# Kernel tuning notes

Measured on AMD Instinct MI355X. Metric: run time of the kernel, lower is better.

## Reference

```python
import jax, jax.numpy as jnp
import numpy as np

N = 200000
C_IN = 128
C_OUT = 256
MID = C_OUT // 4  # bottleneck expansion = 4
K = 27            # 3x3x3 octree neighborhood
EPS = 1e-3


def setup_inputs() -> dict:
    key = jax.random.key(0)
    ks = jax.random.split(key, 8)
    x = jax.random.normal(ks[0], (N, C_IN), dtype=jnp.float32)
    neigh = jax.random.randint(ks[1], (N, K), 0, N, dtype=jnp.int32)
    w1 = jax.random.normal(ks[2], (C_IN, MID), dtype=jnp.float32) / np.sqrt(C_IN)
    w2 = jax.random.normal(ks[3], (K, MID, MID), dtype=jnp.float32) / np.sqrt(K * MID)
    w3 = jax.random.normal(ks[4], (MID, C_OUT), dtype=jnp.float32) / np.sqrt(MID)
    wp = jax.random.normal(ks[5], (C_IN, C_OUT), dtype=jnp.float32) / np.sqrt(C_IN)
    g1 = jnp.ones((MID,), jnp.float32);  b1 = jnp.zeros((MID,), jnp.float32)
    g2 = jnp.ones((MID,), jnp.float32);  b2 = jnp.zeros((MID,), jnp.float32)
    g3 = jnp.ones((C_OUT,), jnp.float32); b3 = jnp.zeros((C_OUT,), jnp.float32)
    gp = jnp.ones((C_OUT,), jnp.float32); bp = jnp.zeros((C_OUT,), jnp.float32)
    return {"x": x, "neigh": neigh, "depth": 6,
            "w1": w1, "g1": g1, "b1": b1,
            "w2": w2, "g2": g2, "b2": b2,
            "w3": w3, "g3": g3, "b3": b3,
            "wp": wp, "gp": gp, "bp": bp}


def _bn(h, g, b):
    # BatchNorm1d over node dim (training-mode batch stats, population var)
    m = jnp.mean(h, axis=0)
    v = jnp.var(h, axis=0)
    return (h - m) * jax.lax.rsqrt(v + EPS) * g + b


def reference(x, neigh, depth, w1, g1, b1, w2, g2, b2, w3, g3, b3, wp, gp, bp):
    # conv_bn_relu1: 1x1x1 octree conv (per-node linear) + BN + ReLU
    h = jax.nn.relu(_bn(x @ w1, g1, b1))           # [N, MID]
    # conv_bn_relu2: 3x3x3 octree conv = gather 27 neighbors + contract
    hn = h[neigh]                                   # [N, 27, MID] irregular gather
    h = jnp.einsum('nkc,kco->no', hn, w2)           # [N, MID]
    h = jax.nn.relu(_bn(h, g2, b2))
    # conv3 + bn3
    h = _bn(h @ w3, g3, b3)                         # [N, C_OUT]
    # projection branch
    p = _bn(x @ wp, gp, bp)                         # [N, C_OUT]
    return jax.nn.relu(h + p)
```

## Files before the change

kernel.cpp:

```cpp
#include <hip/hip_runtime.h>


typedef __bf16 bf16_8 __attribute__((ext_vector_type(8)));
typedef float f32x4 __attribute__((ext_vector_type(4)));

#define NN 200000
#define NBLK 3125

#define OFF_WA    (size_t)0
#define OFF_W3S   (size_t)81920
#define OFF_W2S   (size_t)114688
#define OFF_Y1    (size_t)335872
#define OFF_P1    (size_t)25935872
#define OFF_P2    (size_t)57935872
#define OFF_Y2    (size_t)64335872
#define OFF_H2B   (size_t)89935872
#define OFF_P3    (size_t)115535872
#define OFF_COEF  (size_t)141135872
#define OFF_PA1   (size_t)141142016
#define OFF_PA2   (size_t)141462016
#define OFF_PA3   (size_t)141526016


#define GLDS(gptr, lptr) __builtin_amdgcn_global_load_lds( \
    (const __attribute__((address_space(1))) unsigned int*)(gptr), \
    (__attribute__((address_space(3))) unsigned int*)(lptr), 16, 0, 0)

__global__ void k_prep(const float* __restrict__ w1, const float* __restrict__ w2,
                       const float* __restrict__ w3, const float* __restrict__ wp,
                       __bf16* __restrict__ wA, __bf16* __restrict__ w2S,
                       __bf16* __restrict__ w3S) {
    int i = blockIdx.x * 256 + threadIdx.x;
    if (i < 40960) {
        int j = i & 7, ln = (i >> 3) & 63, ks = (i >> 9) & 3, nt = i >> 11;
        int r = ks * 32 + (ln >> 4) * 8 + j;
        if (nt < 4) wA[i] = (__bf16)w1[r * 64 + nt * 16 + (ln & 15)];
        else        wA[i] = (__bf16)wp[r * 256 + (nt - 4) * 16 + (ln & 15)];
    }
    if (i < 16384) {
        int j = i & 7, ln = (i >> 3) & 63, ks = (i >> 9) & 1, nt = i >> 10;
        int r = ks * 32 + (ln >> 4) * 8 + j;
        w3S[i] = (__bf16)w3[r * 256 + nt * 16 + (ln & 15)];
    }
    if (i < 110592) {
        int j = i & 7, ln = (i >> 3) & 63, ks = (i >> 9) & 1, nt = (i >> 10) & 3, k = i >> 12;
        int c = ks * 32 + (ln >> 4) * 8 + j;
        int o = nt * 16 + (ln & 15);
        w2S[i] = (__bf16)w2[(k * 64 + c) * 64 + o];
    }
}

__global__ __launch_bounds__(256) void k1(const float* __restrict__ x,
                                          const __bf16* __restrict__ wA,
                                          __bf16* __restrict__ y1,
                                          float* __restrict__ p1) {
    __shared__ __align__(16) __bf16 bs[20480];
    __shared__ __align__(16) __bf16 yl[64][72];
    int blk = blockIdx.x, tid = threadIdx.x;
    int wave = tid >> 6, lane = tid & 63, l15 = lane & 15, lg = lane >> 4;

#pragma unroll
    for (int r = 0; r < 10; r++) {
        const char* g = (const char*)wA + r * 4096 + wave * 1024 + lane * 16;
        char* l = (char*)bs + r * 4096 + wave * 1024;
        GLDS(g, l);
    }

    int row = blk * 64 + wave * 16 + l15;
    const float* xr = x + (size_t)row * 128 + lg * 8;
    bf16_8 a[4];
#pragma unroll
    for (int ks = 0; ks < 4; ks++) {
        float4 f0 = *(const float4*)(xr + ks * 32);
        float4 f1 = *(const float4*)(xr + ks * 32 + 4);
        bf16_8 t;
        t[0] = (__bf16)f0.x; t[1] = (__bf16)f0.y; t[2] = (__bf16)f0.z; t[3] = (__bf16)f0.w;
        t[4] = (__bf16)f1.x; t[5] = (__bf16)f1.y; t[6] = (__bf16)f1.z; t[7] = (__bf16)f1.w;
        a[ks] = t;
    }

    f32x4 acc[20];
#pragma unroll
    for (int nt = 0; nt < 20; nt++) acc[nt] = (f32x4){0.f, 0.f, 0.f, 0.f};

    __syncthreads();
#pragma unroll
    for (int nt = 0; nt < 10; nt++) {
#pragma unroll
        for (int ks = 0; ks < 4; ks++) {
            bf16_8 b = *(const bf16_8*)(bs + ((nt * 4 + ks) * 64 + lane) * 8);
            acc[nt] = __builtin_amdgcn_mfma_f32_16x16x32_bf16(a[ks], b, acc[nt], 0, 0, 0);
        }
    }
    __syncthreads();

#pragma unroll
    for (int r = 0; r < 10; r++) {
        const char* g = (const char*)wA + 40960 + r * 4096 + wave * 1024 + lane * 16;
        char* l = (char*)bs + r * 4096 + wave * 1024;
        GLDS(g, l);
    }
#pragma unroll
    for (int nt = 0; nt < 4; nt++)
#pragma unroll
        for (int r4 = 0; r4 < 4; r4++)
            yl[wave * 16 + lg * 4 + r4][nt * 16 + l15] = (__bf16)acc[nt][r4];
    __syncthreads();

#pragma unroll
    for (int p = 0; p < 2; p++) {
        int rr = p * 32 + (tid >> 3), c8 = tid & 7;
        bf16_8 v = *(const bf16_8*)&yl[rr][c8 * 8];
        *(bf16_8*)(y1 + (size_t)(blk * 64 + rr) * 64 + c8 * 8) = v;
    }

#pragma unroll
    for (int nt = 10; nt < 20; nt++) {
#pragma unroll
        for (int ks = 0; ks < 4; ks++) {
            bf16_8 b = *(const bf16_8*)(bs + (((nt - 10) * 4 + ks) * 64 + lane) * 8);
            acc[nt] = __builtin_amdgcn_mfma_f32_16x16x32_bf16(a[ks], b, acc[nt], 0, 0, 0);
        }
    }

    float* prow = p1 + ((size_t)blk * 4 + wave) * 640;
#pragma unroll
    for (int nt = 0; nt < 20; nt++) {
        float s = 0.f, q = 0.f;
#pragma unroll
        for (int r4 = 0; r4 < 4; r4++) { float v = acc[nt][r4]; s += v; q += v * v; }
        s += __shfl_xor(s, 16); s += __shfl_xor(s, 32);
        q += __shfl_xor(q, 16); q += __shfl_xor(q, 32);
        if (lane < 16) { prow[nt * 16 + l15] = s; prow[320 + nt * 16 + l15] = q; }
    }
}

__global__ void k_red(const float* __restrict__ part, float* __restrict__ outp,
                      int nrows, int chunk) {
    int width = blockDim.x;
    int b = blockIdx.x, t = threadIdx.x;
    int r0 = b * chunk, r1 = r0 + chunk;
    if (r1 > nrows) r1 = nrows;
    float s = 0.f;
    for (int r = r0; r < r1; r++) s += part[(size_t)r * width + t];
    outp[(size_t)b * width + t] = s;
}

__global__ void k_fin(const float* __restrict__ psum, const float* __restrict__ psq,
                      int nrows, int rowstride,
                      const float* __restrict__ g, const float* __restrict__ b,
                      float* __restrict__ s_out, float* __restrict__ t_out,
                      const float* __restrict__ fsp, const float* __restrict__ ftp) {
    int c = blockIdx.x;
    float s = 0.f, q = 0.f;
    for (int r = threadIdx.x; r < nrows; r += blockDim.x) {
        size_t o = (size_t)r * rowstride + c;
        s += psum[o]; q += psq[o];
    }
#pragma unroll
    for (int off = 32; off; off >>= 1) { s += __shfl_xor(s, off); q += __shfl_xor(q, off); }
    __shared__ float ls[4], lq[4];
    int wv = threadIdx.x >> 6;
    if ((threadIdx.x & 63) == 0) { ls[wv] = s; lq[wv] = q; }
    __syncthreads();
    if (threadIdx.x == 0) {
        s = ls[0] + ls[1] + ls[2] + ls[3];
        q = lq[0] + lq[1] + lq[2] + lq[3];
        float m = s * (1.f / (float)NN);
        float v = q * (1.f / (float)NN) - m * m;
        float rs = rsqrtf(v + 1e-3f);
        float sc = g[c] * rs;
        float tb = b[c] - m * sc;
        if (fsp) { sc = sc / fsp[c]; tb = tb + ftp[c]; }
        s_out[c] = sc; t_out[c] = tb;
    }
}

__global__ __launch_bounds__(256) void k3(const int* __restrict__ neigh,
                                          const __bf16* __restrict__ y1,
                                          const __bf16* __restrict__ w2S,
                                          const float* __restrict__ coef,
                                          __bf16* __restrict__ y2,
                                          float* __restrict__ p2) {
    __shared__ int nl[64 * 27];
    __shared__ __align__(16) __bf16 bsb[2][4096];

    int blk = blockIdx.x, tid = threadIdx.x;
    int wave = tid >> 6, lane = tid & 63, l15 = lane & 15, lg = lane >> 4;

    for (int i = tid; i < 64 * 27; i += 256) nl[i] = neigh[(size_t)blk * (64 * 27) + i];

    float s0[8], t0[8], s1c[8], t1c[8];
#pragma unroll
    for (int j = 0; j < 8; j++) {
        int c = lg * 8 + j;
        s0[j]  = coef[c];       t0[j]  = coef[64 + c];
        s1c[j] = coef[32 + c];  t1c[j] = coef[96 + c];
    }

#pragma unroll
    for (int r = 0; r < 2; r++) {
        const char* g = (const char*)w2S + r * 4096 + wave * 1024 + lane * 16;
        char* l = (char*)&bsb[0][0] + r * 4096 + wave * 1024;
        GLDS(g, l);
    }
    __syncthreads();

    int row27 = (wave * 16 + l15) * 27;
    int idx0 = nl[row27];
    const __bf16* hp0 = y1 + (size_t)idx0 * 64 + lg * 8;
    bf16_8 r0 = *(const bf16_8*)(hp0);
    bf16_8 r1 = *(const bf16_8*)(hp0 + 32);
    bf16_8 a0, a1;
#pragma unroll
    for (int j = 0; j < 8; j++) {
        a0[j] = (__bf16)fmaxf((float)r0[j] * s0[j] + t0[j], 0.f);
        a1[j] = (__bf16)fmaxf((float)r1[j] * s1c[j] + t1c[j], 0.f);
    }

    f32x4 acc[4];
#pragma unroll
    for (int nt = 0; nt < 4; nt++) acc[nt] = (f32x4){0.f, 0.f, 0.f, 0.f};

    int cur = 0;
    for (int k = 0; k < 27; k++) {
        int kn = (k + 1 < 27) ? k + 1 : 26;
        int idxn = nl[row27 + kn];
        const __bf16* hpn = y1 + (size_t)idxn * 64 + lg * 8;
        bf16_8 rn0 = *(const bf16_8*)(hpn);
        bf16_8 rn1 = *(const bf16_8*)(hpn + 32);
#pragma unroll
        for (int r = 0; r < 2; r++) {
            const char* g = (const char*)w2S + (size_t)kn * 8192 + r * 4096 + wave * 1024 + lane * 16;
            char* l = (char*)&bsb[cur ^ 1][0] + r * 4096 + wave * 1024;
            GLDS(g, l);
        }
        const __bf16* bb = &bsb[cur][0];
#pragma unroll
        for (int nt = 0; nt < 4; nt++) {
            bf16_8 b0 = *(const bf16_8*)(bb + ((nt * 2 + 0) * 64 + lane) * 8);
            bf16_8 b1 = *(const bf16_8*)(bb + ((nt * 2 + 1) * 64 + lane) * 8);
            acc[nt] = __builtin_amdgcn_mfma_f32_16x16x32_bf16(a0, b0, acc[nt], 0, 0, 0);
            acc[nt] = __builtin_amdgcn_mfma_f32_16x16x32_bf16(a1, b1, acc[nt], 0, 0, 0);
        }
        __syncthreads();
#pragma unroll
        for (int j = 0; j < 8; j++) {
            a0[j] = (__bf16)fmaxf((float)rn0[j] * s0[j] + t0[j], 0.f);
            a1[j] = (__bf16)fmaxf((float)rn1[j] * s1c[j] + t1c[j], 0.f);
        }
        cur ^= 1;
    }

#pragma unroll
    for (int nt = 0; nt < 4; nt++)
#pragma unroll
        for (int r4 = 0; r4 < 4; r4++) {
            int gr = blk * 64 + wave * 16 + lg * 4 + r4;
            y2[(size_t)gr * 64 + nt * 16 + l15] = (__bf16)acc[nt][r4];
        }

    float* prow = p2 + ((size_t)blk * 4 + wave) * 128;
#pragma unroll
    for (int nt = 0; nt < 4; nt++) {
        float s = 0.f, q = 0.f;
#pragma unroll
        for (int r4 = 0; r4 < 4; r4++) { float v = acc[nt][r4]; s += v; q += v * v; }
        s += __shfl_xor(s, 16); s += __shfl_xor(s, 32);
        q += __shfl_xor(q, 16); q += __shfl_xor(q, 32);
        if (lane < 16) { prow[nt * 16 + l15] = s; prow[64 + nt * 16 + l15] = q; }
    }
}

__global__ __launch_bounds__(256) void k5(const __bf16* __restrict__ y2,
                                          const float* __restrict__ coef,
                                          const __bf16* __restrict__ w3S,
                                          __bf16* __restrict__ h2b,
                                          float* __restrict__ p3) {
    int blk = blockIdx.x;
    int wave = threadIdx.x >> 6, lane = threadIdx.x & 63;
    int l15 = lane & 15, lg = lane >> 4;
    int row = blk * 64 + wave * 16 + l15;

    bf16_8 a[2];
#pragma unroll
    for (int ks = 0; ks < 2; ks++) {
        bf16_8 v = *(const bf16_8*)(y2 + (size_t)row * 64 + ks * 32 + lg * 8);
        bf16_8 t;
#pragma unroll
        for (int j = 0; j < 8; j++) {
            int c = ks * 32 + lg * 8 + j;
            float f = (float)v[j] * coef[128 + c] + coef[192 + c];
            t[j] = (__bf16)fmaxf(f, 0.f);
        }
        a[ks] = t;
        *(bf16_8*)(h2b + (size_t)row * 64 + ks * 32 + lg * 8) = t;
    }

    f32x4 acc[16];
#pragma unroll
    for (int nt = 0; nt < 16; nt++) acc[nt] = (f32x4){0.f, 0.f, 0.f, 0.f};

#pragma unroll
    for (int nt = 0; nt < 16; nt++) {
        bf16_8 b0 = *(const bf16_8*)(w3S + ((nt * 2 + 0) * 64 + lane) * 8);
        bf16_8 b1 = *(const bf16_8*)(w3S + ((nt * 2 + 1) * 64 + lane) * 8);
        acc[nt] = __builtin_amdgcn_mfma_f32_16x16x32_bf16(a[0], b0, acc[nt], 0, 0, 0);
        acc[nt] = __builtin_amdgcn_mfma_f32_16x16x32_bf16(a[1], b1, acc[nt], 0, 0, 0);
    }

    float* prow = p3 + ((size_t)blk * 4 + wave) * 512;
#pragma unroll
    for (int nt = 0; nt < 16; nt++) {
        float s = 0.f, q = 0.f;
#pragma unroll
        for (int r4 = 0; r4 < 4; r4++) { float v = acc[nt][r4]; s += v; q += v * v; }
        s += __shfl_xor(s, 16); s += __shfl_xor(s, 32);
        q += __shfl_xor(q, 16); q += __shfl_xor(q, 32);
        if (lane < 16) { prow[nt * 16 + l15] = s; prow[256 + nt * 16 + l15] = q; }
    }
}

__global__ __launch_bounds__(256) void k7(const float* __restrict__ x,
                                          const __bf16* __restrict__ h2b,
                                          const __bf16* __restrict__ w3S,
                                          const __bf16* __restrict__ wA,
                                          const float* __restrict__ coef,
                                          float* __restrict__ out) {
    __shared__ __align__(16) char smem[49152];
    int blk = blockIdx.x, tid = threadIdx.x;
    int wave = tid >> 6, lane = tid & 63, l15 = lane & 15, lg = lane >> 4;
    int row = blk * 64 + wave * 16 + l15;

    const __bf16* bsw3 = (const __bf16*)smem;
    const __bf16* bswp = (const __bf16*)(smem + 16384);
    float* el = (float*)smem;

    const __bf16* hp = h2b + (size_t)row * 64 + lg * 8;
    bf16_8 ah0 = *(const bf16_8*)hp;
    bf16_8 ah1 = *(const bf16_8*)(hp + 32);
    const float* xr = x + (size_t)row * 128 + lg * 8;
    bf16_8 ax[4];
#pragma unroll
    for (int ks = 0; ks < 4; ks++) {
        float4 f0 = *(const float4*)(xr + ks * 32);
        float4 f1 = *(const float4*)(xr + ks * 32 + 4);
        bf16_8 t;
        t[0] = (__bf16)f0.x; t[1] = (__bf16)f0.y; t[2] = (__bf16)f0.z; t[3] = (__bf16)f0.w;
        t[4] = (__bf16)f1.x; t[5] = (__bf16)f1.y; t[6] = (__bf16)f1.z; t[7] = (__bf16)f1.w;
        ax[ks] = t;
    }

#pragma unroll
    for (int h = 0; h < 2; h++) {
#pragma unroll
        for (int r = 0; r < 4; r++) {
            const char* g = (const char*)w3S + h * 16384 + r * 4096 + wave * 1024 + lane * 16;
            char* l = smem + r * 4096 + wave * 1024;
            GLDS(g, l);
        }
#pragma unroll
        for (int r = 0; r < 8; r++) {
            const char* g = (const char*)wA + (4 + h * 8) * 4096 + r * 4096 + wave * 1024 + lane * 16;
            char* l = smem + 16384 + r * 4096 + wave * 1024;
            GLDS(g, l);
        }
        __syncthreads();

        f32x4 acc[8];
#pragma unroll
        for (int nt = 0; nt < 8; nt++) acc[nt] = (f32x4){0.f, 0.f, 0.f, 0.f};

#pragma unroll
        for (int nt = 0; nt < 8; nt++) {
            bf16_8 b0 = *(const bf16_8*)(bsw3 + ((nt * 2 + 0) * 64 + lane) * 8);
            bf16_8 b1 = *(const bf16_8*)(bsw3 + ((nt * 2 + 1) * 64 + lane) * 8);
            acc[nt] = __builtin_amdgcn_mfma_f32_16x16x32_bf16(ah0, b0, acc[nt], 0, 0, 0);
            acc[nt] = __builtin_amdgcn_mfma_f32_16x16x32_bf16(ah1, b1, acc[nt], 0, 0, 0);
        }
#pragma unroll
        for (int nt = 0; nt < 8; nt++) acc[nt] *= coef[768 + h * 128 + nt * 16 + l15];
#pragma unroll
        for (int nt = 0; nt < 8; nt++) {
#pragma unroll
            for (int ks = 0; ks < 4; ks++) {
                bf16_8 b = *(const bf16_8*)(bswp + ((nt * 4 + ks) * 64 + lane) * 8);
                acc[nt] = __builtin_amdgcn_mfma_f32_16x16x32_bf16(ax[ks], b, acc[nt], 0, 0, 0);
            }
        }
        __syncthreads();

#pragma unroll
        for (int nt = 0; nt < 8; nt++) {
            int gc = h * 128 + nt * 16 + l15;
            float cs = coef[256 + gc], cb = coef[1280 + gc];
#pragma unroll
            for (int r4 = 0; r4 < 4; r4++)
                el[(wave * 16 + lg * 4 + r4) * 132 + nt * 16 + l15] =
                    fmaxf(acc[nt][r4] * cs + cb, 0.f);
        }
        __syncthreads();
#pragma unroll
        for (int p = 0; p < 8; p++) {
            int rr = p * 8 + (tid >> 5), c4 = tid & 31;
            float4 v = *(const float4*)&el[rr * 132 + c4 * 4];
            *(float4*)(out + (size_t)(blk * 64 + rr) * 256 + h * 128 + c4 * 4) = v;
        }
        __syncthreads();
    }
}

extern "C" void kernel_launch(void* const* d_in, const int* in_sizes, int n_in,
                              void* d_out, int out_size, void* d_ws, size_t ws_size,
                              hipStream_t stream) {
    const float* x     = (const float*)d_in[0];
    const int*   neigh = (const int*)d_in[1];
    const float* w1 = (const float*)d_in[3];
    const float* g1 = (const float*)d_in[4];
    const float* b1 = (const float*)d_in[5];
    const float* w2 = (const float*)d_in[6];
    const float* g2 = (const float*)d_in[7];
    const float* b2 = (const float*)d_in[8];
    const float* w3 = (const float*)d_in[9];
    const float* g3 = (const float*)d_in[10];
    const float* b3 = (const float*)d_in[11];
    const float* wp = (const float*)d_in[12];
    const float* gp = (const float*)d_in[13];
    const float* bp = (const float*)d_in[14];
    float* out = (float*)d_out;

    char* ws = (char*)d_ws;
    __bf16* wA  = (__bf16*)(ws + OFF_WA);
    __bf16* w3S = (__bf16*)(ws + OFF_W3S);
    __bf16* w2S = (__bf16*)(ws + OFF_W2S);
    __bf16* y1  = (__bf16*)(ws + OFF_Y1);
    __bf16* y2  = (__bf16*)(ws + OFF_Y2);
    __bf16* h2b = (__bf16*)(ws + OFF_H2B);
    float* p1   = (float*)(ws + OFF_P1);
    float* p2   = (float*)(ws + OFF_P2);
    float* p3   = (float*)(ws + OFF_P3);
    float* coef = (float*)(ws + OFF_COEF);
    float* pA1  = (float*)(ws + OFF_PA1);
    float* pA2  = (float*)(ws + OFF_PA2);
    float* pA3  = (float*)(ws + OFF_PA3);

    k_prep<<<432, 256, 0, stream>>>(w1, w2, w3, wp, wA, w2S, w3S);

    k1<<<NBLK, 256, 0, stream>>>(x, wA, y1, p1);
    k_red<<<125, 640, 0, stream>>>(p1, pA1, 12500, 100);
    k_fin<<<64, 256, 0, stream>>>(pA1, pA1 + 320, 125, 640, g1, b1,
                                  coef + 0, coef + 64, nullptr, nullptr);
    k_fin<<<256, 256, 0, stream>>>(pA1 + 64, pA1 + 384, 125, 640, gp, bp,
                                   coef + 256, coef + 512, nullptr, nullptr);

    k3<<<NBLK, 256, 0, stream>>>(neigh, y1, w2S, coef, y2, p2);
    k_red<<<125, 128, 0, stream>>>(p2, pA2, 12500, 100);
    k_fin<<<64, 256, 0, stream>>>(pA2, pA2 + 64, 125, 128, g2, b2,
                                  coef + 128, coef + 192, nullptr, nullptr);

    k5<<<NBLK, 256, 0, stream>>>(y2, coef, w3S, h2b, p3);
    k_red<<<125, 512, 0, stream>>>(p3, pA3, 12500, 100);
    k_fin<<<256, 256, 0, stream>>>(pA3, pA3 + 256, 125, 512, g3, b3,
                                   coef + 768, coef + 1280, coef + 256, coef + 512);

    k7<<<NBLK, 256, 0, stream>>>(x, h2b, w3S, wA, coef, out);
}
```

Baseline: 619.8 us.

## Derive BN3 statistics from Gram matrix of h2 and precompute BN1-ReLU activations

BN3 statistics are now computed algebraically: a persistent kernel accumulates the 64x64 Gram matrix h2ᵀh2 and column sums with MFMA, and per-output mean and variance come from w3ᵀMw3. This replaces the full 256-wide conv3 pass, its h2b write and the large partial-sum reduction. BN1+ReLU is applied once in a new elementwise pass so the 27-way gather in k3 reads ready activations, with a two-deep prefetch. k7 recomputes BN2+ReLU from y2 on the fly. The trade-off is an extra pass over y1 and a variance formula more exposed to cancellation.

```diff
diff --git a/kernel.cpp b/kernel.cpp
--- a/kernel.cpp
+++ b/kernel.cpp
@@ -14,12 +14,14 @@
 #define OFF_P1    (size_t)25935872
 #define OFF_P2    (size_t)57935872
 #define OFF_Y2    (size_t)64335872
-#define OFF_H2B   (size_t)89935872
-#define OFF_P3    (size_t)115535872
-#define OFF_COEF  (size_t)141135872
-#define OFF_PA1   (size_t)141142016
-#define OFF_PA2   (size_t)141462016
-#define OFF_PA3   (size_t)141526016
+#define OFF_H1    (size_t)89935872
+#define OFF_COEF  (size_t)115535872
+#define OFF_PA1   (size_t)115542016
+#define OFF_PA2   (size_t)115862016
+#define OFF_MP    (size_t)115926016
+#define OFF_CSP   (size_t)124314624
+#define OFF_MM    (size_t)124445696
+#define OFF_CS    (size_t)124462080
 
 
 #define GLDS(gptr, lptr) __builtin_amdgcn_global_load_lds( \
@@ -149,8 +151,7 @@
 __global__ void k_fin(const float* __restrict__ psum, const float* __restrict__ psq,
                       int nrows, int rowstride,
                       const float* __restrict__ g, const float* __restrict__ b,
-                      float* __restrict__ s_out, float* __restrict__ t_out,
-                      const float* __restrict__ fsp, const float* __restrict__ ftp) {
+                      float* __restrict__ s_out, float* __restrict__ t_out) {
     int c = blockIdx.x;
     float s = 0.f, q = 0.f;
     for (int r = threadIdx.x; r < nrows; r += blockDim.x) {
@@ -170,16 +171,28 @@
         float v = q * (1.f / (float)NN) - m * m;
         float rs = rsqrtf(v + 1e-3f);
         float sc = g[c] * rs;
-        float tb = b[c] - m * sc;
-        if (fsp) { sc = sc / fsp[c]; tb = tb + ftp[c]; }
-        s_out[c] = sc; t_out[c] = tb;
-    }
+        s_out[c] = sc; t_out[c] = b[c] - m * sc;
+    }
+}
+
+__global__ __launch_bounds__(256) void k_h1(const __bf16* __restrict__ y1,
+                                            const float* __restrict__ coef,
+                                            __bf16* __restrict__ h1) {
+    int i = blockIdx.x * 256 + threadIdx.x;
+    int c0 = (i * 8) & 63;
+    bf16_8 v = *(const bf16_8*)(y1 + (size_t)i * 8);
+    bf16_8 o;
+#pragma unroll
+    for (int j = 0; j < 8; j++) {
+        float f = (float)v[j] * coef[c0 + j] + coef[64 + c0 + j];
+        o[j] = (__bf16)fmaxf(f, 0.f);
+    }
+    *(bf16_8*)(h1 + (size_t)i * 8) = o;
 }
 
 __global__ __launch_bounds__(256) void k3(const int* __restrict__ neigh,
-                                          const __bf16* __restrict__ y1,
+                                          const __bf16* __restrict__ h1,
                                           const __bf16* __restrict__ w2S,
-                                          const float* __restrict__ coef,
                                           __bf16* __restrict__ y2,
                                           float* __restrict__ p2) {
     __shared__ int nl[64 * 27];
@@ -188,15 +201,7 @@
     int blk = blockIdx.x, tid = threadIdx.x;
     int wave = tid >> 6, lane = tid & 63, l15 = lane & 15, lg = lane >> 4;
 
-    for (int i = tid; i < 64 * 27; i += 256) nl[i] = neigh[(size_t)blk * (64 * 27) + i];
-
-    float s0[8], t0[8], s1c[8], t1c[8];
-#pragma unroll
-    for (int j = 0; j < 8; j++) {
-        int c = lg * 8 + j;
-        s0[j]  = coef[c];       t0[j]  = coef[64 + c];
-        s1c[j] = coef[32 + c];  t1c[j] = coef[96 + c];
-    }
+    for (int i = tid; i < 64 * 27; i += 256) nl[i] = neigh[(size_t)blk * 1728 + i];
 
 #pragma unroll
     for (int r = 0; r < 2; r++) {
@@ -207,16 +212,11 @@
     __syncthreads();
 
     int row27 = (wave * 16 + l15) * 27;
-    int idx0 = nl[row27];
-    const __bf16* hp0 = y1 + (size_t)idx0 * 64 + lg * 8;
-    bf16_8 r0 = *(const bf16_8*)(hp0);
-    bf16_8 r1 = *(const bf16_8*)(hp0 + 32);
-    bf16_8 a0, a1;
-#pragma unroll
-    for (int j = 0; j < 8; j++) {
-        a0[j] = (__bf16)fmaxf((float)r0[j] * s0[j] + t0[j], 0.f);
-        a1[j] = (__bf16)fmaxf((float)r1[j] * s1c[j] + t1c[j], 0.f);
-    }
+    int i0 = nl[row27 + 0], i1 = nl[row27 + 1];
+    const __bf16* hp0 = h1 + (size_t)i0 * 64 + lg * 8;
+    const __bf16* hp1 = h1 + (size_t)i1 * 64 + lg * 8;
+    bf16_8 c0 = *(const bf16_8*)hp0, c1 = *(const bf16_8*)(hp0 + 32);
+    bf16_8 n0 = *(const bf16_8*)hp1, n1 = *(const bf16_8*)(hp1 + 32);
 
     f32x4 acc[4];
 #pragma unroll
@@ -224,31 +224,31 @@
 
     int cur = 0;
     for (int k = 0; k < 27; k++) {
-        int kn = (k + 1 < 27) ? k + 1 : 26;
-        int idxn = nl[row27 + kn];
-        const __bf16* hpn = y1 + (size_t)idxn * 64 + lg * 8;
-        bf16_8 rn0 = *(const bf16_8*)(hpn);
-        bf16_8 rn1 = *(const bf16_8*)(hpn + 32);
-#pragma unroll
-        for (int r = 0; r < 2; r++) {
-            const char* g = (const char*)w2S + (size_t)kn * 8192 + r * 4096 + wave * 1024 + lane * 16;
-            char* l = (char*)&bsb[cur ^ 1][0] + r * 4096 + wave * 1024;
-            GLDS(g, l);
+        if (k < 26) {
+#pragma unroll
+            for (int r = 0; r < 2; r++) {
+                const char* g = (const char*)w2S + (size_t)(k + 1) * 8192 + r * 4096 + wave * 1024 + lane * 16;
+                char* l = (char*)&bsb[cur ^ 1][0] + r * 4096 + wave * 1024;
+                GLDS(g, l);
+            }
+        }
+        bf16_8 p0 = c0, p1 = c1;
+        if (k < 25) {
+            int i2 = nl[row27 + k + 2];
+            const __bf16* hp2 = h1 + (size_t)i2 * 64 + lg * 8;
+            p0 = *(const bf16_8*)hp2;
+            p1 = *(const bf16_8*)(hp2 + 32);
         }
         const __bf16* bb = &bsb[cur][0];
 #pragma unroll
         for (int nt = 0; nt < 4; nt++) {
             bf16_8 b0 = *(const bf16_8*)(bb + ((nt * 2 + 0) * 64 + lane) * 8);
             bf16_8 b1 = *(const bf16_8*)(bb + ((nt * 2 + 1) * 64 + lane) * 8);
-            acc[nt] = __builtin_amdgcn_mfma_f32_16x16x32_bf16(a0, b0, acc[nt], 0, 0, 0);
-            acc[nt] = __builtin_amdgcn_mfma_f32_16x16x32_bf16(a1, b1, acc[nt], 0, 0, 0);
-        }
-        __syncthreads();
-#pragma unroll
-        for (int j = 0; j < 8; j++) {
-            a0[j] = (__bf16)fmaxf((float)rn0[j] * s0[j] + t0[j], 0.f);
-            a1[j] = (__bf16)fmaxf((float)rn1[j] * s1c[j] + t1c[j], 0.f);
-        }
+            acc[nt] = __builtin_amdgcn_mfma_f32_16x16x32_bf16(c0, b0, acc[nt], 0, 0, 0);
+            acc[nt] = __builtin_amdgcn_mfma_f32_16x16x32_bf16(c1, b1, acc[nt], 0, 0, 0);
+        }
+        __syncthreads();
+        c0 = n0; c1 = n1; n0 = p0; n1 = p1;
         cur ^= 1;
     }
 
@@ -272,57 +272,125 @@
     }
 }
 
-__global__ __launch_bounds__(256) void k5(const __bf16* __restrict__ y2,
-                                          const float* __restrict__ coef,
-                                          const __bf16* __restrict__ w3S,
-                                          __bf16* __restrict__ h2b,
-                                          float* __restrict__ p3) {
-    int blk = blockIdx.x;
-    int wave = threadIdx.x >> 6, lane = threadIdx.x & 63;
-    int l15 = lane & 15, lg = lane >> 4;
-    int row = blk * 64 + wave * 16 + l15;
-
-    bf16_8 a[2];
-#pragma unroll
-    for (int ks = 0; ks < 2; ks++) {
-        bf16_8 v = *(const bf16_8*)(y2 + (size_t)row * 64 + ks * 32 + lg * 8);
-        bf16_8 t;
+__global__ __launch_bounds__(256) void k5m(const __bf16* __restrict__ y2,
+                                           const float* __restrict__ coef,
+                                           float* __restrict__ Mpart,
+                                           float* __restrict__ cspart) {
+    __shared__ __align__(16) __bf16 hl[64][80];
+    int blk = blockIdx.x, tid = threadIdx.x;
+    int wave = tid >> 6, lane = tid & 63, l15 = lane & 15, lg = lane >> 4;
+
+    float s0[8], t0[8], s1[8], t1[8];
+#pragma unroll
+    for (int j = 0; j < 8; j++) {
+        int c = lg * 8 + j;
+        s0[j] = coef[128 + c];      t0[j] = coef[192 + c];
+        s1[j] = coef[160 + c];      t1[j] = coef[224 + c];
+    }
+    bf16_8 ones;
+#pragma unroll
+    for (int j = 0; j < 8; j++) ones[j] = (__bf16)1.0f;
+
+    f32x4 acc[4], acc1;
+#pragma unroll
+    for (int nt = 0; nt < 4; nt++) acc[nt] = (f32x4){0.f, 0.f, 0.f, 0.f};
+    acc1 = (f32x4){0.f, 0.f, 0.f, 0.f};
+
+    for (int t = blk; t < NBLK; t += 512) {
+        const __bf16* yp = y2 + ((size_t)t * 64 + wave * 16 + l15) * 64 + lg * 8;
+        bf16_8 v0 = *(const bf16_8*)yp, v1 = *(const bf16_8*)(yp + 32);
+        bf16_8 h0, h2;
 #pragma unroll
         for (int j = 0; j < 8; j++) {
-            int c = ks * 32 + lg * 8 + j;
-            float f = (float)v[j] * coef[128 + c] + coef[192 + c];
-            t[j] = (__bf16)fmaxf(f, 0.f);
-        }
-        a[ks] = t;
-        *(bf16_8*)(h2b + (size_t)row * 64 + ks * 32 + lg * 8) = t;
-    }
-
-    f32x4 acc[16];
-#pragma unroll
-    for (int nt = 0; nt < 16; nt++) acc[nt] = (f32x4){0.f, 0.f, 0.f, 0.f};
-
-#pragma unroll
-    for (int nt = 0; nt < 16; nt++) {
-        bf16_8 b0 = *(const bf16_8*)(w3S + ((nt * 2 + 0) * 64 + lane) * 8);
-        bf16_8 b1 = *(const bf16_8*)(w3S + ((nt * 2 + 1) * 64 + lane) * 8);
-        acc[nt] = __builtin_amdgcn_mfma_f32_16x16x32_bf16(a[0], b0, acc[nt], 0, 0, 0);
-        acc[nt] = __builtin_amdgcn_mfma_f32_16x16x32_bf16(a[1], b1, acc[nt], 0, 0, 0);
-    }
-
-    float* prow = p3 + ((size_t)blk * 4 + wave) * 512;
-#pragma unroll
-    for (int nt = 0; nt < 16; nt++) {
-        float s = 0.f, q = 0.f;
-#pragma unroll
-        for (int r4 = 0; r4 < 4; r4++) { float v = acc[nt][r4]; s += v; q += v * v; }
-        s += __shfl_xor(s, 16); s += __shfl_xor(s, 32);
-        q += __shfl_xor(q, 16); q += __shfl_xor(q, 32);
-        if (lane < 16) { prow[nt * 16 + l15] = s; prow[256 + nt * 16 + l15] = q; }
+            h0[j] = (__bf16)fmaxf((float)v0[j] * s0[j] + t0[j], 0.f);
+            h2[j] = (__bf16)fmaxf((float)v1[j] * s1[j] + t1[j], 0.f);
+        }
+        __syncthreads();
+        *(bf16_8*)&hl[wave * 16 + l15][lg * 8] = h0;
+        *(bf16_8*)&hl[wave * 16 + l15][32 + lg * 8] = h2;
+        __syncthreads();
+
+        bf16_8 fa[2], fb[4][2];
+#pragma unroll
+        for (int ks = 0; ks < 2; ks++)
+#pragma unroll
+            for (int j = 0; j < 8; j++)
+                fa[ks][j] = hl[ks * 32 + lg * 8 + j][wave * 16 + l15];
+#pragma unroll
+        for (int nt = 0; nt < 4; nt++)
+#pragma unroll
+            for (int ks = 0; ks < 2; ks++)
+#pragma unroll
+                for (int j = 0; j < 8; j++)
+                    fb[nt][ks][j] = hl[ks * 32 + lg * 8 + j][nt * 16 + l15];
+
+#pragma unroll
+        for (int nt = 0; nt < 4; nt++)
+#pragma unroll
+            for (int ks = 0; ks < 2; ks++)
+                acc[nt] = __builtin_amdgcn_mfma_f32_16x16x32_bf16(fa[ks], fb[nt][ks], acc[nt], 0, 0, 0);
+#pragma unroll
+        for (int ks = 0; ks < 2; ks++)
+            acc1 = __builtin_amdgcn_mfma_f32_16x16x32_bf16(ones, fa[ks], acc1, 0, 0, 0);
+    }
+
+#pragma unroll
+    for (int nt = 0; nt < 4; nt++)
+#pragma unroll
+        for (int r4 = 0; r4 < 4; r4++)
+            Mpart[((size_t)blk * 64 + wave * 16 + lg * 4 + r4) * 64 + nt * 16 + l15] = acc[nt][r4];
+    if (lg == 0) cspart[blk * 64 + wave * 16 + l15] = acc1[0];
+}
+
+__global__ void k_redM(const float* __restrict__ Mpart, const float* __restrict__ cspart,
+                       float* __restrict__ Mout, float* __restrict__ csout) {
+    int b = blockIdx.x, t = threadIdx.x;
+    if (b < 16) {
+        int col = b * 256 + t;
+        float s = 0.f;
+        for (int r = 0; r < 512; r++) s += Mpart[(size_t)r * 4096 + col];
+        Mout[col] = s;
+    } else if (t < 64) {
+        float s = 0.f;
+        for (int r = 0; r < 512; r++) s += cspart[r * 64 + t];
+        csout[t] = s;
+    }
+}
+
+__global__ void k_fin3(const float* __restrict__ M, const float* __restrict__ cs,
+                       const float* __restrict__ w3, const float* __restrict__ g3,
+                       const float* __restrict__ b3, float* __restrict__ coef) {
+    int o = blockIdx.x, t = threadIdx.x;
+    __shared__ float w3l[64];
+    if (t < 64) w3l[t] = (float)(__bf16)w3[t * 256 + o];
+    __syncthreads();
+    int c = t >> 2, c0 = (t & 3) * 16;
+    float q = 0.f;
+#pragma unroll
+    for (int j = 0; j < 16; j++) q += M[c * 64 + c0 + j] * w3l[c0 + j];
+    q *= w3l[c];
+    float m = (t < 64) ? cs[t] * w3l[t] : 0.f;
+#pragma unroll
+    for (int off = 32; off; off >>= 1) { q += __shfl_xor(q, off); m += __shfl_xor(m, off); }
+    __shared__ float lq[4], lm[4];
+    int wv = t >> 6;
+    if ((t & 63) == 0) { lq[wv] = q; lm[wv] = m; }
+    __syncthreads();
+    if (t == 0) {
+        float Q = lq[0] + lq[1] + lq[2] + lq[3];
+        float S = lm[0] + lm[1] + lm[2] + lm[3];
+        float mean = S * (1.f / (float)NN);
+        float var = Q * (1.f / (float)NN) - mean * mean;
+        float rs = rsqrtf(var + 1e-3f);
+        float s3 = g3[o] * rs;
+        float t3 = b3[o] - mean * s3;
+        coef[768 + o] = s3 / coef[256 + o];
+        coef[1280 + o] = t3 + coef[512 + o];
     }
 }
 
 __global__ __launch_bounds__(256) void k7(const float* __restrict__ x,
-                                          const __bf16* __restrict__ h2b,
+                                          const __bf16* __restrict__ y2,
                                           const __bf16* __restrict__ w3S,
                                           const __bf16* __restrict__ wA,
                                           const float* __restrict__ coef,
@@ -336,9 +404,15 @@
     const __bf16* bswp = (const __bf16*)(smem + 16384);
     float* el = (float*)smem;
 
-    const __bf16* hp = h2b + (size_t)row * 64 + lg * 8;
-    bf16_8 ah0 = *(const bf16_8*)hp;
-    bf16_8 ah1 = *(const bf16_8*)(hp + 32);
+    const __bf16* yp = y2 + (size_t)row * 64 + lg * 8;
+    bf16_8 v0 = *(const bf16_8*)yp, v1 = *(const bf16_8*)(yp + 32);
+    bf16_8 ah0, ah1;
+#pragma unroll
+    for (int j = 0; j < 8; j++) {
+        int c = lg * 8 + j;
+        ah0[j] = (__bf16)fmaxf((float)v0[j] * coef[128 + c] + coef[192 + c], 0.f);
+        ah1[j] = (__bf16)fmaxf((float)v1[j] * coef[160 + c] + coef[224 + c], 0.f);
+    }
     const float* xr = x + (size_t)row * 128 + lg * 8;
     bf16_8 ax[4];
 #pragma unroll
@@ -435,33 +509,33 @@
     __bf16* w2S = (__bf16*)(ws + OFF_W2S);
     __bf16* y1  = (__bf16*)(ws + OFF_Y1);
     __bf16* y2  = (__bf16*)(ws + OFF_Y2);
-    __bf16* h2b = (__bf16*)(ws + OFF_H2B);
+    __bf16* h1  = (__bf16*)(ws + OFF_H1);
     float* p1   = (float*)(ws + OFF_P1);
     float* p2   = (float*)(ws + OFF_P2);
-    float* p3   = (float*)(ws + OFF_P3);
     float* coef = (float*)(ws + OFF_COEF);
     float* pA1  = (float*)(ws + OFF_PA1);
     float* pA2  = (float*)(ws + OFF_PA2);
-    float* pA3  = (float*)(ws + OFF_PA3);
+    float* Mp   = (float*)(ws + OFF_MP);
+    float* csp  = (float*)(ws + OFF_CSP);
+    float* Mm   = (float*)(ws + OFF_MM);
+    float* csv  = (float*)(ws + OFF_CS);
 
     k_prep<<<432, 256, 0, stream>>>(w1, w2, w3, wp, wA, w2S, w3S);
 
     k1<<<NBLK, 256, 0, stream>>>(x, wA, y1, p1);
     k_red<<<125, 640, 0, stream>>>(p1, pA1, 12500, 100);
-    k_fin<<<64, 256, 0, stream>>>(pA1, pA1 + 320, 125, 640, g1, b1,
-                                  coef + 0, coef + 64, nullptr, nullptr);
-    k_fin<<<256, 256, 0, stream>>>(pA1 + 64, pA1 + 384, 125, 640, gp, bp,
-                                   coef + 256, coef + 512, nullptr, nullptr);
-
-    k3<<<NBLK, 256, 0, stream>>>(neigh, y1, w2S, coef, y2, p2);
+    k_fin<<<64, 256, 0, stream>>>(pA1, pA1 + 320, 125, 640, g1, b1, coef + 0, coef + 64);
+    k_fin<<<256, 256, 0, stream>>>(pA1 + 64, pA1 + 384, 125, 640, gp, bp, coef + 256, coef + 512);
+
+    k_h1<<<6250, 256, 0, stream>>>(y1, coef, h1);
+
+    k3<<<NBLK, 256, 0, stream>>>(neigh, h1, w2S, y2, p2);
     k_red<<<125, 128, 0, stream>>>(p2, pA2, 12500, 100);
-    k_fin<<<64, 256, 0, stream>>>(pA2, pA2 + 64, 125, 128, g2, b2,
-                                  coef + 128, coef + 192, nullptr, nullptr);
-
-    k5<<<NBLK, 256, 0, stream>>>(y2, coef, w3S, h2b, p3);
-    k_red<<<125, 512, 0, stream>>>(p3, pA3, 12500, 100);
-    k_fin<<<256, 256, 0, stream>>>(pA3, pA3 + 256, 125, 512, g3, b3,
-                                   coef + 768, coef + 1280, coef + 256, coef + 512);
-
-    k7<<<NBLK, 256, 0, stream>>>(x, h2b, w3S, wA, coef, out);
-}
+    k_fin<<<64, 256, 0, stream>>>(pA2, pA2 + 64, 125, 128, g2, b2, coef + 128, coef + 192);
+
+    k5m<<<512, 256, 0, stream>>>(y2, coef, Mp, csp);
+    k_redM<<<17, 256, 0, stream>>>(Mp, csp, Mm, csv);
+    k_fin3<<<256, 256, 0, stream>>>(Mm, csv, w3, g3, b3, coef);
+
+    k7<<<NBLK, 256, 0, stream>>>(x, y2, w3S, wA, coef, out);
+}
```

Result: faster. 588.4 us (-5.1%).
